# Kernel tuning notes

Hardware: AMD Instinct MI355X
Metric: run time of the kernel (lower is better)

The kernel has to match this reference:

```python
import jax, jax.numpy as jnp
import numpy as np

B = 256
NUM_ROUTES = 32 * 6 * 6  # 1152
NUM_CAPS = 10
OUT_CH = 16
IN_CH = 8


def squash(x, axis=-1):
    sq = jnp.sum(x * x, axis=axis, keepdims=True)
    return sq * x / ((1.0 + sq) * jnp.sqrt(sq))


def conv2d(x, w, b, stride):
    y = jax.lax.conv_general_dilated(
        x, w, window_strides=(stride, stride), padding='VALID',
        dimension_numbers=('NCHW', 'OIHW', 'NCHW'))
    return y + b[None, :, None, None]


def setup_inputs() -> dict:
    key = jax.random.key(0)
    ks = jax.random.split(key, 12)
    data = jax.random.normal(ks[0], (B, 1, 28, 28), dtype=jnp.float32)
    conv1_w = jax.random.normal(ks[1], (256, 1, 9, 9), dtype=jnp.float32) * 0.1
    conv1_b = jax.random.normal(ks[2], (256,), dtype=jnp.float32) * 0.01
    # 8 primary-capsule convs, each 256->32, k9 s2 (stacked)
    pc_w = jax.random.normal(ks[3], (8, 32, 256, 9, 9), dtype=jnp.float32) * 0.02
    pc_b = jax.random.normal(ks[4], (8, 32), dtype=jnp.float32) * 0.01
    # DigitCaps routing weights (torch.randn init)
    W_dc = jax.random.normal(ks[5], (NUM_ROUTES, NUM_CAPS, OUT_CH, IN_CH), dtype=jnp.float32)
    dec_w1 = jax.random.normal(ks[6], (160, 512), dtype=jnp.float32) * 0.05
    dec_b1 = jnp.zeros((512,), dtype=jnp.float32)
    dec_w2 = jax.random.normal(ks[7], (512, 1024), dtype=jnp.float32) * 0.05
    dec_b2 = jnp.zeros((1024,), dtype=jnp.float32)
    dec_w3 = jax.random.normal(ks[8], (1024, 784), dtype=jnp.float32) * 0.05
    dec_b3 = jnp.zeros((784,), dtype=jnp.float32)
    return dict(data=data, conv1_w=conv1_w, conv1_b=conv1_b, pc_w=pc_w, pc_b=pc_b,
                W_dc=W_dc, dec_w1=dec_w1, dec_b1=dec_b1, dec_w2=dec_w2,
                dec_b2=dec_b2, dec_w3=dec_w3, dec_b3=dec_b3)


def capsnet_forward(data, conv1_w, conv1_b, pc_w, pc_b, W_dc,
                    dec_w1, dec_b1, dec_w2, dec_b2, dec_w3, dec_b3):
    bsz = data.shape[0]
    # ConvLayer: [B,1,28,28] -> [B,256,20,20]
    x = jax.nn.relu(conv2d(data, conv1_w, conv1_b, 1))
    # PrimaryCaps: 8 independent convs fused into one 256-out conv then split
    # [B,256,6,6] viewed as [B,8,32,6,6] matches torch.stack(u, dim=1)
    u = conv2d(x, pc_w.reshape(256, 256, 9, 9), pc_b.reshape(256), 2)
    u = u.reshape(bsz, NUM_ROUTES, IN_CH)  # [B,1152,8]
    u = squash(u)
    # DigitCaps: u_hat[b,r,c,o] = sum_i W[r,c,o,i] * u[b,r,i]
    u_hat = jnp.einsum('rcoi,bri->brco', W_dc, u)  # [B,1152,10,16]
    b_ij = jnp.zeros((NUM_ROUTES, NUM_CAPS), dtype=u_hat.dtype)
    num_iterations = 3
    v = None
    for it in range(num_iterations):
        c_ij = jax.nn.softmax(b_ij, axis=0)            # softmax over routes
        s_j = jnp.einsum('rc,brco->bco', c_ij, u_hat)  # [B,10,16]
        v = squash(s_j, axis=-1)
        if it < num_iterations - 1:
            a_ij = jnp.einsum('brco,bco->rc', u_hat, v) / bsz  # mean over batch
            b_ij = b_ij + a_ij
    output = v[..., None]  # [B,10,16,1]
    # Decoder
    classes = jnp.sqrt(jnp.sum(output ** 2, axis=2))   # [B,10,1]
    classes = jax.nn.softmax(classes, axis=0)          # softmax over batch (as in source)
    idx = jnp.argmax(classes, axis=1)[:, 0]            # [B]
    masked = jnp.eye(NUM_CAPS, dtype=output.dtype)[idx]  # [B,10]
    t = (output * masked[:, :, None, None]).reshape(bsz, -1)  # [B,160]
    h = jax.nn.relu(t @ dec_w1 + dec_b1)
    h = jax.nn.relu(h @ dec_w2 + dec_b2)
    recon = jax.nn.sigmoid(h @ dec_w3 + dec_b3).reshape(bsz, 1, 28, 28)
    return output, recon, masked


def reference(data, conv1_w, conv1_b, pc_w, pc_b, W_dc,
              dec_w1, dec_b1, dec_w2, dec_b2, dec_w3, dec_b3):
    return capsnet_forward(data, conv1_w, conv1_b, pc_w, pc_b, W_dc,
                           dec_w1, dec_b1, dec_w2, dec_b2, dec_w3, dec_b3)
```

## Files before the change

### kernel.cpp

```cpp
#include <hip/hip_runtime.h>
#include <math.h>


typedef __attribute__((ext_vector_type(8))) short short8;
typedef __attribute__((ext_vector_type(4))) float f32x4;

__device__ __forceinline__ unsigned short f2bf(float x) {
  unsigned int u = __float_as_uint(x);
  unsigned int r = (u + 0x7fffu + ((u >> 16) & 1u)) >> 16;
  return (unsigned short)r;
}
__device__ __forceinline__ float bf2f(unsigned short h) {
  return __uint_as_float(((unsigned int)h) << 16);
}
__device__ __forceinline__ void gload16(const void* g, void* l) {
  __builtin_amdgcn_global_load_lds(
      (const __attribute__((address_space(1))) unsigned int*)g,
      (__attribute__((address_space(3))) unsigned int*)l, 16, 0, 0);
}
__device__ __forceinline__ float dot8(const float* w, float4 a, float4 b) {
  return w[0]*a.x + w[1]*a.y + w[2]*a.z + w[3]*a.w +
         w[4]*b.x + w[5]*b.y + w[6]*b.z + w[7]*b.w;
}

__global__ __launch_bounds__(320) void conv1_kernel(
    const float* __restrict__ data, const float* __restrict__ w1,
    const float* __restrict__ b1, unsigned short* __restrict__ xh,
    unsigned short* __restrict__ xl)
{
  const int bid = blockIdx.x;
  const int b   = bid >> 2;
  const int cog = bid & 3;
  __shared__ float img[784];
  __shared__ float wsm[81][64];
  const int t = threadIdx.x;
  for (int i = t; i < 784; i += 320) img[i] = data[b * 784 + i];
  for (int i = t; i < 64 * 81; i += 320) {
    int col = i / 81, k = i % 81;
    wsm[k][col] = w1[(cog * 64 + col) * 81 + k];
  }
  __syncthreads();
  const int cg = t & 15;
  const int oy = t >> 4;
  const int co0 = cog * 64 + cg * 4;
  float acc[4][20];
  #pragma unroll
  for (int i = 0; i < 4; i++) {
    float bv = b1[co0 + i];
    #pragma unroll
    for (int j = 0; j < 20; j++) acc[i][j] = bv;
  }
  for (int ky = 0; ky < 9; ky++) {
    float xr[28];
    const float4* rp = reinterpret_cast<const float4*>(&img[(oy + ky) * 28]);
    #pragma unroll
    for (int q = 0; q < 7; q++) {
      float4 v4 = rp[q];
      xr[q*4+0] = v4.x; xr[q*4+1] = v4.y; xr[q*4+2] = v4.z; xr[q*4+3] = v4.w;
    }
    #pragma unroll
    for (int kx = 0; kx < 9; kx++) {
      float4 wv = *reinterpret_cast<const float4*>(&wsm[ky * 9 + kx][cg * 4]);
      #pragma unroll
      for (int ox = 0; ox < 20; ox++) {
        float xv = xr[ox + kx];
        acc[0][ox] = fmaf(xv, wv.x, acc[0][ox]);
        acc[1][ox] = fmaf(xv, wv.y, acc[1][ox]);
        acc[2][ox] = fmaf(xv, wv.z, acc[2][ox]);
        acc[3][ox] = fmaf(xv, wv.w, acc[3][ox]);
      }
    }
  }
  #pragma unroll
  for (int ox = 0; ox < 20; ox++) {
    ushort4 hv, lv;
    float v0 = fmaxf(acc[0][ox], 0.f), v1 = fmaxf(acc[1][ox], 0.f);
    float v2 = fmaxf(acc[2][ox], 0.f), v3 = fmaxf(acc[3][ox], 0.f);
    hv.x = f2bf(v0); lv.x = f2bf(v0 - bf2f(hv.x));
    hv.y = f2bf(v1); lv.y = f2bf(v1 - bf2f(hv.y));
    hv.z = f2bf(v2); lv.z = f2bf(v2 - bf2f(hv.z));
    hv.w = f2bf(v3); lv.w = f2bf(v3 - bf2f(hv.w));
    const int pix = (b * 20 + oy) * 20 + ox;
    *(ushort4*)(xh + pix * 256 + co0) = hv;
    *(ushort4*)(xl + pix * 256 + co0) = lv;
  }
}

__global__ void wprep(const float* __restrict__ pw, unsigned short* __restrict__ wh,
                      unsigned short* __restrict__ wl)
{
  const int co = blockIdx.x;
  const int t  = threadIdx.x;
  __shared__ float slab[20736];
  for (int i = t; i < 20736; i += 256) slab[i] = pw[co * 20736 + i];
  __syncthreads();
  for (int k = 0; k < 81; k++) {
    float x = slab[t * 81 + k];
    unsigned short h = f2bf(x);
    wh[(k * 256 + co) * 256 + t] = h;
    wl[(k * 256 + co) * 256 + t] = f2bf(x - bf2f(h));
  }
}

__global__ __launch_bounds__(256, 1) void conv2_mfma(
    const unsigned short* __restrict__ xh, const unsigned short* __restrict__ xl,
    const unsigned short* __restrict__ wh, const unsigned short* __restrict__ wl,
    float* __restrict__ part)
{
  extern __shared__ char lds[];
  const int t   = threadIdx.x;
  const int blk = blockIdx.x;
  const int mt  = blk % 72;
  const int kg  = blk / 72;
  const int m0  = mt * 128;
  const int lane = t & 63;
  const int w    = t >> 6;
  const int l15  = lane & 15, l4 = lane >> 4;
  const int mh   = w >> 1, nh = w & 1;
  const int swz  = l15 & 7;

  const int ib2 = ((t >> 2) ^ (t >> 4)) & 1;
  const int ib1 = ((t >> 1) ^ (t >> 3)) & 1;
  const int ib0 = (t ^ (t >> 2) ^ (t >> 4)) & 1;
  const int g   = (t & ~7) | (ib2 << 2) | (ib1 << 1) | ib0;
  const int ar  = g >> 2;
  const int ach = g & 3;

  auto pixbase = [&](int pix) {
    int ab = pix / 36; int sp = pix - ab * 36;
    int oy = sp / 6;   int ox = sp - oy * 6;
    return ((ab * 20 + 2 * oy) * 20 + 2 * ox) * 256;
  };
  const int abase0 = pixbase(m0 + ar) + ach * 8;
  const int abase1 = pixbase(m0 + ar + 64) + ach * 8;
  const int bofs   = ar * 256 + ach * 8;

  f32x4 acc[4][8];
  #pragma unroll
  for (int i = 0; i < 4; i++)
    #pragma unroll
    for (int j = 0; j < 8; j++) acc[i][j] = (f32x4){0.f, 0.f, 0.f, 0.f};

  const int ky0 = kg * 3;

  auto stage = [&](int buf, int ky, int kx, int ci0) {
    char* base = lds + buf * 49152;
    const int axy = (ky * 20 + kx) * 256 + ci0;
    const int wxy = (ky * 9 + kx) * 65536 + ci0 + bofs;
    gload16(xh + abase0 + axy, base + t * 16);
    gload16(xh + abase1 + axy, base + 4096  + t * 16);
    gload16(xl + abase0 + axy, base + 8192  + t * 16);
    gload16(xl + abase1 + axy, base + 12288 + t * 16);
    const unsigned short* wph = wh + wxy;
    const unsigned short* wpl = wl + wxy;
    char* bh = base + 16384 + t * 16;
    char* bl = base + 32768 + t * 16;
    #pragma unroll
    for (int i = 0; i < 4; i++) {
      gload16(wph + i * 16384, bh + i * 4096);
      gload16(wpl + i * 16384, bl + i * 4096);
    }
  };

  stage(0, ky0, 0, 0);

  int kyn = ky0, kxn = 0, ccn = 0;
  #pragma unroll 1
  for (int s = 0; s < 216; ++s) {
    const int cur = s & 1;
    ccn++;
    if (ccn == 8) { ccn = 0; kxn++; if (kxn == 9) { kxn = 0; kyn++; } }
    if (s < 215) {
      stage(cur ^ 1, kyn, kxn, ccn * 32);
      asm volatile("s_waitcnt vmcnt(12)" ::: "memory");
    } else {
      asm volatile("s_waitcnt vmcnt(0)" ::: "memory");
    }
    asm volatile("s_barrier" ::: "memory");

    char* base = lds + cur * 49152;
    short8 a_h[4], a_l[4];
    #pragma unroll
    for (int mf = 0; mf < 4; mf++) {
      const int row = mh * 64 + mf * 16 + l15;
      const int off = ((((row << 2) | l4) ^ swz) << 4);
      a_h[mf] = *(const short8*)(base + off);
      a_l[mf] = *(const short8*)(base + 8192 + off);
    }
    #pragma unroll
    for (int half = 0; half < 2; half++) {
      short8 b_h[4], b_l[4];
      #pragma unroll
      for (int j = 0; j < 4; j++) {
        const int row = nh * 128 + (half * 4 + j) * 16 + l15;
        const int off = ((((row << 2) | l4) ^ swz) << 4);
        b_h[j] = *(const short8*)(base + 16384 + off);
        b_l[j] = *(const short8*)(base + 32768 + off);
      }
      __builtin_amdgcn_s_setprio(1);
      #pragma unroll
      for (int j = 0; j < 4; j++)
        #pragma unroll
        for (int mf = 0; mf < 4; mf++) {
          f32x4 a = acc[mf][half * 4 + j];
          a = __builtin_amdgcn_mfma_f32_16x16x32_bf16(a_h[mf], b_h[j], a, 0, 0, 0);
          a = __builtin_amdgcn_mfma_f32_16x16x32_bf16(a_l[mf], b_h[j], a, 0, 0, 0);
          a = __builtin_amdgcn_mfma_f32_16x16x32_bf16(a_h[mf], b_l[j], a, 0, 0, 0);
          acc[mf][half * 4 + j] = a;
        }
      __builtin_amdgcn_s_setprio(0);
    }
    asm volatile("s_barrier" ::: "memory");
  }

  float* pout = part + kg * 2359296;
  #pragma unroll
  for (int mf = 0; mf < 4; mf++)
    #pragma unroll
    for (int nf = 0; nf < 8; nf++) {
      const int co = nh * 128 + nf * 16 + l15;
      #pragma unroll
      for (int reg = 0; reg < 4; reg++) {
        const int pix = m0 + mh * 64 + mf * 16 + l4 * 4 + reg;
        const int b  = pix / 36;
        const int sp = pix - b * 36;
        pout[b * 9216 + co * 36 + sp] = acc[mf][nf][reg];
      }
    }
}

__global__ void combine_squash(const float* __restrict__ part,
                               const float* __restrict__ pb,
                               float* __restrict__ uT)
{
  const int id = blockIdx.x * 256 + threadIdx.x;
  const int b = id / 1152;
  const int r = id % 1152;
  const float* p0 = part + b * 9216 + r * 8;
  float v[8];
  #pragma unroll
  for (int i = 0; i < 8; i++) v[i] = p0[i] + p0[2359296 + i] + p0[4718592 + i];
  #pragma unroll
  for (int i = 0; i < 8; i++) v[i] += pb[(r * 8 + i) / 36];
  float sq = 0.f;
  #pragma unroll
  for (int i = 0; i < 8; i++) sq += v[i] * v[i];
  float scale = sq / ((1.f + sq) * sqrtf(sq));
  #pragma unroll
  for (int i = 0; i < 8; i++) uT[(r * 256 + b) * 8 + i] = v[i] * scale;
}

__global__ __launch_bounds__(256) void s_pass(
    const float* __restrict__ uT, const float* __restrict__ Wdc,
    const float* __restrict__ bij, float* __restrict__ spart, int uniform)
{
  const int c  = blockIdx.x % 10;
  const int q  = blockIdx.x / 10;
  const int r0 = q * 18;
  const int t  = threadIdx.x;
  __shared__ float wsm[18 * 128];
  __shared__ float cw[18];
  __shared__ float red[8];

  #pragma unroll
  for (int k = 0; k < 9; k++) {
    int idx = t + k * 256;
    int r = idx >> 7, i = idx & 127;
    wsm[idx] = Wdc[((r0 + r) * 10 + c) * 128 + i];
  }
  if (uniform) {
    if (t < 18) cw[t] = 1.f / 1152.f;
  } else {
    float bv[5]; float m = -1e30f;
    #pragma unroll
    for (int rr = 0; rr < 5; rr++) {
      int r = t + rr * 256;
      bv[rr] = (r < 1152) ? bij[c * 1152 + r] : -1e30f;
      m = fmaxf(m, bv[rr]);
    }
    #pragma unroll
    for (int off = 32; off; off >>= 1) m = fmaxf(m, __shfl_down(m, off, 64));
    if ((t & 63) == 0) red[t >> 6] = m;
    __syncthreads();
    m = fmaxf(fmaxf(red[0], red[1]), fmaxf(red[2], red[3]));
    float ssum = 0.f;
    #pragma unroll
    for (int rr = 0; rr < 5; rr++)
      ssum += (t + rr * 256 < 1152) ? expf(bv[rr] - m) : 0.f;
    #pragma unroll
    for (int off = 32; off; off >>= 1) ssum += __shfl_down(ssum, off, 64);
    if ((t & 63) == 0) red[4 + (t >> 6)] = ssum;
    __syncthreads();
    float inv = 1.f / (red[4] + red[5] + red[6] + red[7]);
    if (t < 18) cw[t] = expf(bij[c * 1152 + r0 + t] - m) * inv;
  }
  __syncthreads();

  const float4* up = (const float4*)(uT + (r0 * 256 + t) * 8);
  float acc[16];
  #pragma unroll
  for (int o = 0; o < 16; o++) acc[o] = 0.f;
  #pragma unroll 1
  for (int r = 0; r < 18; r++) {
    float4 x0 = up[r * 512], x1 = up[r * 512 + 1];
    float cwr = cw[r];
    const float* wr = &wsm[r * 128];
    #pragma unroll
    for (int o = 0; o < 16; o++) {
      const float4 wa = *(const float4*)(wr + o * 8);
      const float4 wb = *(const float4*)(wr + o * 8 + 4);
      acc[o] += cwr * (wa.x*x0.x + wa.y*x0.y + wa.z*x0.z + wa.w*x0.w
                     + wb.x*x1.x + wb.y*x1.y + wb.z*x1.z + wb.w*x1.w);
    }
  }
  float* op = spart + q * 40960 + (t * 10 + c) * 16;
  #pragma unroll
  for (int o = 0; o < 16; o++) op[o] = acc[o];
}

__global__ void reduce_s(const float* __restrict__ spart, float* __restrict__ sbuf)
{
  const int id = blockIdx.x * 256 + threadIdx.x;
  float a = 0.f;
  #pragma unroll 8
  for (int q = 0; q < 64; q++) a += spart[q * 40960 + id];
  sbuf[id] = a;
}

__global__ void squash_nf(const float* __restrict__ s, float* __restrict__ vT)
{
  const int id = blockIdx.x * 256 + threadIdx.x;
  const int b = id / 10, c = id - b * 10;
  const float4* sp = (const float4*)(s + id * 16);
  float4 q0 = sp[0], q1 = sp[1], q2 = sp[2], q3 = sp[3];
  float sq = q0.x*q0.x+q0.y*q0.y+q0.z*q0.z+q0.w*q0.w
           + q1.x*q1.x+q1.y*q1.y+q1.z*q1.z+q1.w*q1.w
           + q2.x*q2.x+q2.y*q2.y+q2.z*q2.z+q2.w*q2.w
           + q3.x*q3.x+q3.y*q3.y+q3.z*q3.z+q3.w*q3.w;
  float scale = sq / ((1.f + sq) * sqrtf(sq));
  float4* vp = (float4*)(vT + (c * 256 + b) * 16);
  vp[0] = make_float4(q0.x*scale, q0.y*scale, q0.z*scale, q0.w*scale);
  vp[1] = make_float4(q1.x*scale, q1.y*scale, q1.z*scale, q1.w*scale);
  vp[2] = make_float4(q2.x*scale, q2.y*scale, q2.z*scale, q2.w*scale);
  vp[3] = make_float4(q3.x*scale, q3.y*scale, q3.z*scale, q3.w*scale);
}

__global__ __launch_bounds__(256) void a_pass(
    const float* __restrict__ uT, const float* __restrict__ W,
    const float* __restrict__ vT, float* __restrict__ bij, int assign)
{
  const int r = blockIdx.x;
  const int t = threadIdx.x;
  __shared__ float wsl[1280];
  __shared__ float lred[4][10];
  for (int i = t; i < 1280; i += 256) wsl[i] = W[r * 1280 + i];
  __syncthreads();
  const float4* up = (const float4*)(uT + (r * 256 + t) * 8);
  float4 ua = up[0], ub = up[1];
  const int lane = t & 63, wid = t >> 6;
  #pragma unroll 1
  for (int c = 0; c < 10; c++) {
    const float* wc = &wsl[c * 128];
    const float4* vp = (const float4*)(vT + (c * 256 + t) * 16);
    float p = 0.f;
    #pragma unroll
    for (int q = 0; q < 4; q++) {
      float4 vq = vp[q];
      p += dot8(wc + (q * 4 + 0) * 8, ua, ub) * vq.x;
      p += dot8(wc + (q * 4 + 1) * 8, ua, ub) * vq.y;
      p += dot8(wc + (q * 4 + 2) * 8, ua, ub) * vq.z;
      p += dot8(wc + (q * 4 + 3) * 8, ua, ub) * vq.w;
    }
    for (int off = 32; off; off >>= 1) p += __shfl_down(p, off, 64);
    if (lane == 0) lred[wid][c] = p;
  }
  __syncthreads();
  if (t < 10) {
    float a = (lred[0][t] + lred[1][t] + lred[2][t] + lred[3][t]) * (1.f / 256.f);
    float o = assign ? 0.f : bij[t * 1152 + r];
    bij[t * 1152 + r] = o + a;
  }
}

__global__ __launch_bounds__(256) void finalize(
    const float* __restrict__ sbuf, float* __restrict__ outp,
    float* __restrict__ maskedo, float* __restrict__ tbuf)
{
  const int b = threadIdx.x;
  __shared__ float nsm[256][10];
  __shared__ float red[8];
  #pragma unroll 1
  for (int c = 0; c < 10; c++) {
    const float4* sp = (const float4*)(sbuf + (b * 10 + c) * 16);
    float4 q0 = sp[0], q1 = sp[1], q2 = sp[2], q3 = sp[3];
    float sq = q0.x*q0.x+q0.y*q0.y+q0.z*q0.z+q0.w*q0.w
             + q1.x*q1.x+q1.y*q1.y+q1.z*q1.z+q1.w*q1.w
             + q2.x*q2.x+q2.y*q2.y+q2.z*q2.z+q2.w*q2.w
             + q3.x*q3.x+q3.y*q3.y+q3.z*q3.z+q3.w*q3.w;
    float scale = sq / ((1.f + sq) * sqrtf(sq));
    float4* op = (float4*)(outp + (b * 10 + c) * 16);
    op[0] = make_float4(q0.x*scale, q0.y*scale, q0.z*scale, q0.w*scale);
    op[1] = make_float4(q1.x*scale, q1.y*scale, q1.z*scale, q1.w*scale);
    op[2] = make_float4(q2.x*scale, q2.y*scale, q2.z*scale, q2.w*scale);
    op[3] = make_float4(q3.x*scale, q3.y*scale, q3.z*scale, q3.w*scale);
    nsm[b][c] = sq / (1.f + sq);
  }
  __syncthreads();
  float sc[10];
  #pragma unroll
  for (int c = 0; c < 10; c++) {
    float x = nsm[b][c];
    float m = x;
    #pragma unroll
    for (int off = 32; off; off >>= 1) m = fmaxf(m, __shfl_down(m, off, 64));
    if ((b & 63) == 0) red[b >> 6] = m;
    __syncthreads();
    m = fmaxf(fmaxf(red[0], red[1]), fmaxf(red[2], red[3]));
    float e = expf(x - m), ss = e;
    #pragma unroll
    for (int off = 32; off; off >>= 1) ss += __shfl_down(ss, off, 64);
    if ((b & 63) == 0) red[4 + (b >> 6)] = ss;
    __syncthreads();
    sc[c] = e / (red[4] + red[5] + red[6] + red[7]);
    __syncthreads();
  }
  int idx = 0; float best = sc[0];
  #pragma unroll
  for (int c = 1; c < 10; c++) if (sc[c] > best) { best = sc[c]; idx = c; }
  #pragma unroll
  for (int c = 0; c < 10; c++) {
    float msk = (c == idx) ? 1.f : 0.f;
    maskedo[b * 10 + c] = msk;
    const float4* op = (const float4*)(outp + (b * 10 + c) * 16);
    float4* tp = (float4*)(tbuf + b * 160 + c * 16);
    #pragma unroll
    for (int qq = 0; qq < 4; qq++) {
      float4 vv = op[qq];
      tp[qq] = make_float4(vv.x * msk, vv.y * msk, vv.z * msk, vv.w * msk);
    }
  }
}

template <int ACT>
__global__ __launch_bounds__(256) void gemm_act(
    const float* __restrict__ A, const float* __restrict__ B,
    const float* __restrict__ bias, float* __restrict__ C, int M, int N, int K)
{
  __shared__ float As[64][17];
  __shared__ float Bs[16][64];
  const int t = threadIdx.x;
  const int tx = t & 15, ty = t >> 4;
  const int m0 = blockIdx.y * 64, n0 = blockIdx.x * 64;
  float acc[4][4] = {};
  for (int kb = 0; kb < K; kb += 16) {
    {
      int row = t >> 2, c4 = (t & 3) * 4;
      float4 av = *(const float4*)(A + (m0 + row) * K + kb + c4);
      As[row][c4+0]=av.x; As[row][c4+1]=av.y; As[row][c4+2]=av.z; As[row][c4+3]=av.w;
    }
    {
      int row = t >> 4, c4 = (t & 15) * 4;
      float4 bv = make_float4(0.f, 0.f, 0.f, 0.f);
      if (n0 + c4 < N) bv = *(const float4*)(B + (kb + row) * N + n0 + c4);
      Bs[row][c4+0]=bv.x; Bs[row][c4+1]=bv.y; Bs[row][c4+2]=bv.z; Bs[row][c4+3]=bv.w;
    }
    __syncthreads();
    #pragma unroll
    for (int kk = 0; kk < 16; kk++) {
      float a_[4], b_[4];
      #pragma unroll
      for (int i = 0; i < 4; i++) a_[i] = As[ty * 4 + i][kk];
      #pragma unroll
      for (int j = 0; j < 4; j++) b_[j] = Bs[kk][tx * 4 + j];
      #pragma unroll
      for (int i = 0; i < 4; i++)
        for (int j = 0; j < 4; j++)
          acc[i][j] = fmaf(a_[i], b_[j], acc[i][j]);
    }
    __syncthreads();
  }
  #pragma unroll
  for (int i = 0; i < 4; i++) {
    int row = m0 + ty * 4 + i;
    #pragma unroll
    for (int j = 0; j < 4; j++) {
      int col = n0 + tx * 4 + j;
      if (col < N) {
        float val = acc[i][j] + bias[col];
        if (ACT == 0) val = val > 0.f ? val : 0.f;
        else          val = 1.f / (1.f + expf(-val));
        C[row * N + col] = val;
      }
    }
  }
}

extern "C" void kernel_launch(void* const* d_in, const int* in_sizes, int n_in,
                              void* d_out, int out_size, void* d_ws, size_t ws_size,
                              hipStream_t stream)
{
  const float* data = (const float*)d_in[0];
  const float* w1   = (const float*)d_in[1];
  const float* b1   = (const float*)d_in[2];
  const float* pw   = (const float*)d_in[3];
  const float* pb   = (const float*)d_in[4];
  const float* Wdc  = (const float*)d_in[5];
  const float* dw1  = (const float*)d_in[6];
  const float* db1  = (const float*)d_in[7];
  const float* dw2  = (const float*)d_in[8];
  const float* db2  = (const float*)d_in[9];
  const float* dw3  = (const float*)d_in[10];
  const float* db3  = (const float*)d_in[11];

  float* out     = (float*)d_out;
  float* outp    = out;
  float* recon   = out + 40960;
  float* maskedo = out + 241664;

  char* wsb = (char*)d_ws;
  unsigned short* x1h = (unsigned short*)(wsb);
  unsigned short* x1l = (unsigned short*)(wsb + 52428800);
  unsigned short* wbh = (unsigned short*)(wsb + 104857600);
  unsigned short* wbl = (unsigned short*)(wsb + 115474432);
  float*  part = (float*)(wsb + 126091264);
  float* uT   = (float*)(wsb);
  float* vT   = (float*)(wsb + 9437184);
  float* bij  = (float*)(wsb + 9601024);
  float* sbuf = (float*)(wsb + 9647104);
  float* spart= (float*)(wsb + 9810944);
  float* tbuf = (float*)(wsb + 20296704);
  float* h1   = (float*)(wsb + 20460544);
  float* h2   = (float*)(wsb + 20984832);

  conv1_kernel<<<1024, 320, 0, stream>>>(data, w1, b1, x1h, x1l);
  wprep<<<256, 256, 0, stream>>>(pw, wbh, wbl);
  conv2_mfma<<<216, 256, 98304, stream>>>(x1h, x1l, wbh, wbl, part);
  combine_squash<<<1152, 256, 0, stream>>>(part, pb, uT);

  s_pass<<<640, 256, 0, stream>>>(uT, Wdc, bij, spart, 1);
  reduce_s<<<160, 256, 0, stream>>>(spart, sbuf);
  squash_nf<<<10, 256, 0, stream>>>(sbuf, vT);
  a_pass<<<1152, 256, 0, stream>>>(uT, Wdc, vT, bij, 1);
  s_pass<<<640, 256, 0, stream>>>(uT, Wdc, bij, spart, 0);
  reduce_s<<<160, 256, 0, stream>>>(spart, sbuf);
  squash_nf<<<10, 256, 0, stream>>>(sbuf, vT);
  a_pass<<<1152, 256, 0, stream>>>(uT, Wdc, vT, bij, 0);
  s_pass<<<640, 256, 0, stream>>>(uT, Wdc, bij, spart, 0);
  reduce_s<<<160, 256, 0, stream>>>(spart, sbuf);
  finalize<<<1, 256, 0, stream>>>(sbuf, outp, maskedo, tbuf);

  gemm_act<0><<<dim3(8, 4),  256, 0, stream>>>(tbuf, dw1, db1, h1,    256, 512,  160);
  gemm_act<0><<<dim3(16, 4), 256, 0, stream>>>(h1,   dw2, db2, h2,    256, 1024, 512);
  gemm_act<1><<<dim3(13, 4), 256, 0, stream>>>(h2,   dw3, db3, recon, 256, 784,  1024);
}
```

Before: 779.8 us.

## Retile conv2 MFMA to 64-row tiles with direct-register weight loads

The primary-capsule conv kernel now uses 64-pixel M tiles, which doubles the grid to 432 blocks. Each wave owns 64 output channels and loads its weight fragments straight from global memory into registers, instead of staging them through LDS. The weight prep lays weights out per 32-channel slab to match. Only activations go through a triple-buffered LDS ring, with one barrier per step. The aim is better occupancy and less LDS traffic. The trade-off is more global/L2 weight reads and exposed load latency. The reduce and squash kernels of routing are also fused into one kernel using shuffle reductions, removing two launches.

```diff
diff --git a/kernel.cpp b/kernel.cpp
--- a/kernel.cpp
+++ b/kernel.cpp
@@ -94,134 +94,115 @@
   __shared__ float slab[20736];
   for (int i = t; i < 20736; i += 256) slab[i] = pw[co * 20736 + i];
   __syncthreads();
+  const int cc = t >> 5, ci5 = t & 31;
   for (int k = 0; k < 81; k++) {
     float x = slab[t * 81 + k];
     unsigned short h = f2bf(x);
-    wh[(k * 256 + co) * 256 + t] = h;
-    wl[(k * 256 + co) * 256 + t] = f2bf(x - bf2f(h));
-  }
-}
-
-__global__ __launch_bounds__(256, 1) void conv2_mfma(
+    int dst = ((k * 8 + cc) * 256 + co) * 32 + ci5;
+    wh[dst] = h;
+    wl[dst] = f2bf(x - bf2f(h));
+  }
+}
+
+__global__ __launch_bounds__(256) void conv2_mfma(
     const unsigned short* __restrict__ xh, const unsigned short* __restrict__ xl,
     const unsigned short* __restrict__ wh, const unsigned short* __restrict__ wl,
     float* __restrict__ part)
 {
-  extern __shared__ char lds[];
+  __shared__ char lds[24576];
   const int t   = threadIdx.x;
   const int blk = blockIdx.x;
-  const int mt  = blk % 72;
-  const int kg  = blk / 72;
-  const int m0  = mt * 128;
+  const int mt  = blk % 144;
+  const int kg  = blk / 144;
+  const int m0  = mt * 64;
   const int lane = t & 63;
   const int w    = t >> 6;
   const int l15  = lane & 15, l4 = lane >> 4;
-  const int mh   = w >> 1, nh = w & 1;
-  const int swz  = l15 & 7;
 
   const int ib2 = ((t >> 2) ^ (t >> 4)) & 1;
   const int ib1 = ((t >> 1) ^ (t >> 3)) & 1;
   const int ib0 = (t ^ (t >> 2) ^ (t >> 4)) & 1;
   const int g   = (t & ~7) | (ib2 << 2) | (ib1 << 1) | ib0;
-  const int ar  = g >> 2;
-  const int ach = g & 3;
-
-  auto pixbase = [&](int pix) {
-    int ab = pix / 36; int sp = pix - ab * 36;
-    int oy = sp / 6;   int ox = sp - oy * 6;
-    return ((ab * 20 + 2 * oy) * 20 + 2 * ox) * 256;
+  const int ar  = g >> 2, ach = g & 3;
+  const int apix = m0 + ar;
+  const int ab  = apix / 36;
+  const int asp = apix - ab * 36;
+  const int aoy = asp / 6;
+  const int aox = asp - aoy * 6;
+  const int abase = ((ab * 20 + 2 * aoy) * 20 + 2 * aox) * 256 + ach * 8;
+
+  const int bofs = (w * 64 + l15) * 32 + l4 * 8;
+
+  f32x4 acc[4][4];
+  #pragma unroll
+  for (int i = 0; i < 4; i++)
+    #pragma unroll
+    for (int j = 0; j < 4; j++) acc[i][j] = (f32x4){0.f, 0.f, 0.f, 0.f};
+
+  const int ky0 = kg * 3;
+
+  auto stageA = [&](int buf, int axy) {
+    char* base = lds + buf * 8192;
+    gload16(xh + abase + axy, base + t * 16);
+    gload16(xl + abase + axy, base + 4096 + t * 16);
   };
-  const int abase0 = pixbase(m0 + ar) + ach * 8;
-  const int abase1 = pixbase(m0 + ar + 64) + ach * 8;
-  const int bofs   = ar * 256 + ach * 8;
-
-  f32x4 acc[4][8];
-  #pragma unroll
-  for (int i = 0; i < 4; i++)
-    #pragma unroll
-    for (int j = 0; j < 8; j++) acc[i][j] = (f32x4){0.f, 0.f, 0.f, 0.f};
-
-  const int ky0 = kg * 3;
-
-  auto stage = [&](int buf, int ky, int kx, int ci0) {
-    char* base = lds + buf * 49152;
-    const int axy = (ky * 20 + kx) * 256 + ci0;
-    const int wxy = (ky * 9 + kx) * 65536 + ci0 + bofs;
-    gload16(xh + abase0 + axy, base + t * 16);
-    gload16(xh + abase1 + axy, base + 4096  + t * 16);
-    gload16(xl + abase0 + axy, base + 8192  + t * 16);
-    gload16(xl + abase1 + axy, base + 12288 + t * 16);
-    const unsigned short* wph = wh + wxy;
-    const unsigned short* wpl = wl + wxy;
-    char* bh = base + 16384 + t * 16;
-    char* bl = base + 32768 + t * 16;
-    #pragma unroll
-    for (int i = 0; i < 4; i++) {
-      gload16(wph + i * 16384, bh + i * 4096);
-      gload16(wpl + i * 16384, bl + i * 4096);
-    }
-  };
-
-  stage(0, ky0, 0, 0);
-
-  int kyn = ky0, kxn = 0, ccn = 0;
+
+  stageA(0, (ky0 * 20) * 256);
+  int kyc = ky0, kxc = 0, ccc = 0;
   #pragma unroll 1
   for (int s = 0; s < 216; ++s) {
-    const int cur = s & 1;
-    ccn++;
-    if (ccn == 8) { ccn = 0; kxn++; if (kxn == 9) { kxn = 0; kyn++; } }
+    const int slab = ((kyc * 9 + kxc) * 8 + ccc) * 8192;
+    const unsigned short* bhp = wh + slab + bofs;
+    const unsigned short* blp = wl + slab + bofs;
+    short8 b_h[4], b_l[4];
+    #pragma unroll
+    for (int nf = 0; nf < 4; nf++) {
+      b_h[nf] = *(const short8*)(bhp + nf * 512);
+      b_l[nf] = *(const short8*)(blp + nf * 512);
+    }
+    ccc++;
+    if (ccc == 8) { ccc = 0; kxc++; if (kxc == 9) { kxc = 0; kyc++; } }
     if (s < 215) {
-      stage(cur ^ 1, kyn, kxn, ccn * 32);
-      asm volatile("s_waitcnt vmcnt(12)" ::: "memory");
+      stageA((s + 1) % 3, (kyc * 20 + kxc) * 256 + ccc * 32);
+      asm volatile("s_waitcnt vmcnt(10)" ::: "memory");
     } else {
-      asm volatile("s_waitcnt vmcnt(0)" ::: "memory");
+      asm volatile("s_waitcnt vmcnt(8)" ::: "memory");
     }
     asm volatile("s_barrier" ::: "memory");
 
-    char* base = lds + cur * 49152;
+    char* base = lds + (s % 3) * 8192;
     short8 a_h[4], a_l[4];
     #pragma unroll
     for (int mf = 0; mf < 4; mf++) {
-      const int row = mh * 64 + mf * 16 + l15;
-      const int off = ((((row << 2) | l4) ^ swz) << 4);
+      const int row = mf * 16 + l15;
+      const int off = ((((row << 2) | l4) ^ (l15 & 7)) << 4);
       a_h[mf] = *(const short8*)(base + off);
-      a_l[mf] = *(const short8*)(base + 8192 + off);
-    }
-    #pragma unroll
-    for (int half = 0; half < 2; half++) {
-      short8 b_h[4], b_l[4];
+      a_l[mf] = *(const short8*)(base + 4096 + off);
+    }
+    __builtin_amdgcn_s_setprio(1);
+    #pragma unroll
+    for (int nf = 0; nf < 4; nf++)
       #pragma unroll
-      for (int j = 0; j < 4; j++) {
-        const int row = nh * 128 + (half * 4 + j) * 16 + l15;
-        const int off = ((((row << 2) | l4) ^ swz) << 4);
-        b_h[j] = *(const short8*)(base + 16384 + off);
-        b_l[j] = *(const short8*)(base + 32768 + off);
+      for (int mf = 0; mf < 4; mf++) {
+        f32x4 a = acc[mf][nf];
+        a = __builtin_amdgcn_mfma_f32_16x16x32_bf16(a_h[mf], b_h[nf], a, 0, 0, 0);
+        a = __builtin_amdgcn_mfma_f32_16x16x32_bf16(a_l[mf], b_h[nf], a, 0, 0, 0);
+        a = __builtin_amdgcn_mfma_f32_16x16x32_bf16(a_h[mf], b_l[nf], a, 0, 0, 0);
+        acc[mf][nf] = a;
       }
-      __builtin_amdgcn_s_setprio(1);
-      #pragma unroll
-      for (int j = 0; j < 4; j++)
-        #pragma unroll
-        for (int mf = 0; mf < 4; mf++) {
-          f32x4 a = acc[mf][half * 4 + j];
-          a = __builtin_amdgcn_mfma_f32_16x16x32_bf16(a_h[mf], b_h[j], a, 0, 0, 0);
-          a = __builtin_amdgcn_mfma_f32_16x16x32_bf16(a_l[mf], b_h[j], a, 0, 0, 0);
-          a = __builtin_amdgcn_mfma_f32_16x16x32_bf16(a_h[mf], b_l[j], a, 0, 0, 0);
-          acc[mf][half * 4 + j] = a;
-        }
-      __builtin_amdgcn_s_setprio(0);
-    }
-    asm volatile("s_barrier" ::: "memory");
+    __builtin_amdgcn_s_setprio(0);
+    asm volatile("s_waitcnt lgkmcnt(0)" ::: "memory");
   }
 
   float* pout = part + kg * 2359296;
   #pragma unroll
   for (int mf = 0; mf < 4; mf++)
     #pragma unroll
-    for (int nf = 0; nf < 8; nf++) {
-      const int co = nh * 128 + nf * 16 + l15;
+    for (int nf = 0; nf < 4; nf++) {
+      const int co = w * 64 + nf * 16 + l15;
       #pragma unroll
       for (int reg = 0; reg < 4; reg++) {
-        const int pix = m0 + mh * 64 + mf * 16 + l4 * 4 + reg;
+        const int pix = m0 + mf * 16 + l4 * 4 + reg;
         const int b  = pix / 36;
         const int sp = pix - b * 36;
         pout[b * 9216 + co * 36 + sp] = acc[mf][nf][reg];
@@ -318,31 +299,21 @@
   for (int o = 0; o < 16; o++) op[o] = acc[o];
 }
 
-__global__ void reduce_s(const float* __restrict__ spart, float* __restrict__ sbuf)
+template <int FINAL>
+__global__ void reduce_squash(const float* __restrict__ spart, float* __restrict__ outb)
 {
   const int id = blockIdx.x * 256 + threadIdx.x;
   float a = 0.f;
   #pragma unroll 8
   for (int q = 0; q < 64; q++) a += spart[q * 40960 + id];
-  sbuf[id] = a;
-}
-
-__global__ void squash_nf(const float* __restrict__ s, float* __restrict__ vT)
-{
-  const int id = blockIdx.x * 256 + threadIdx.x;
-  const int b = id / 10, c = id - b * 10;
-  const float4* sp = (const float4*)(s + id * 16);
-  float4 q0 = sp[0], q1 = sp[1], q2 = sp[2], q3 = sp[3];
-  float sq = q0.x*q0.x+q0.y*q0.y+q0.z*q0.z+q0.w*q0.w
-           + q1.x*q1.x+q1.y*q1.y+q1.z*q1.z+q1.w*q1.w
-           + q2.x*q2.x+q2.y*q2.y+q2.z*q2.z+q2.w*q2.w
-           + q3.x*q3.x+q3.y*q3.y+q3.z*q3.z+q3.w*q3.w;
+  if (FINAL) { outb[id] = a; return; }
+  float sq = a * a;
+  #pragma unroll
+  for (int off = 8; off; off >>= 1) sq += __shfl_xor(sq, off, 16);
   float scale = sq / ((1.f + sq) * sqrtf(sq));
-  float4* vp = (float4*)(vT + (c * 256 + b) * 16);
-  vp[0] = make_float4(q0.x*scale, q0.y*scale, q0.z*scale, q0.w*scale);
-  vp[1] = make_float4(q1.x*scale, q1.y*scale, q1.z*scale, q1.w*scale);
-  vp[2] = make_float4(q2.x*scale, q2.y*scale, q2.z*scale, q2.w*scale);
-  vp[3] = make_float4(q3.x*scale, q3.y*scale, q3.z*scale, q3.w*scale);
+  const int bc = id >> 4, o = id & 15;
+  const int b = bc / 10, c = bc - b * 10;
+  outb[(c * 256 + b) * 16 + o] = a * scale;
 }
 
 __global__ __launch_bounds__(256) void a_pass(
@@ -534,19 +505,17 @@
 
   conv1_kernel<<<1024, 320, 0, stream>>>(data, w1, b1, x1h, x1l);
   wprep<<<256, 256, 0, stream>>>(pw, wbh, wbl);
-  conv2_mfma<<<216, 256, 98304, stream>>>(x1h, x1l, wbh, wbl, part);
+  conv2_mfma<<<432, 256, 0, stream>>>(x1h, x1l, wbh, wbl, part);
   combine_squash<<<1152, 256, 0, stream>>>(part, pb, uT);
 
   s_pass<<<640, 256, 0, stream>>>(uT, Wdc, bij, spart, 1);
-  reduce_s<<<160, 256, 0, stream>>>(spart, sbuf);
-  squash_nf<<<10, 256, 0, stream>>>(sbuf, vT);
+  reduce_squash<0><<<160, 256, 0, stream>>>(spart, vT);
   a_pass<<<1152, 256, 0, stream>>>(uT, Wdc, vT, bij, 1);
   s_pass<<<640, 256, 0, stream>>>(uT, Wdc, bij, spart, 0);
-  reduce_s<<<160, 256, 0, stream>>>(spart, sbuf);
-  squash_nf<<<10, 256, 0, stream>>>(sbuf, vT);
+  reduce_squash<0><<<160, 256, 0, stream>>>(spart, vT);
   a_pass<<<1152, 256, 0, stream>>>(uT, Wdc, vT, bij, 0);
   s_pass<<<640, 256, 0, stream>>>(uT, Wdc, bij, spart, 0);
-  reduce_s<<<160, 256, 0, stream>>>(spart, sbuf);
+  reduce_squash<1><<<160, 256, 0, stream>>>(spart, sbuf);
   finalize<<<1, 256, 0, stream>>>(sbuf, outp, maskedo, tbuf);
 
   gemm_act<0><<<dim3(8, 4),  256, 0, stream>>>(tbuf, dw1, db1, h1,    256, 512,  160);
```

Measured after the change: 692.9 us. 1.13x faster.
